# Optimization experiments

Measured on AMD Instinct MI355X. Metric: run time of the kernel, lower is better.

## Reference

```python
import jax, jax.numpy as jnp
import numpy as np
from jax import lax

PI = 3.141592653589793

def _sobel_kernel(dtype):
    # (2,1,3,3): channel 0 = d/dx (Sobel x), channel 1 = d/dy (Sobel y)
    sx = jnp.array([[-1., 0., 1.], [-2., 0., 2.], [-1., 0., 1.]], dtype=dtype)
    sy = jnp.array([[-1., -2., -1.], [0., 0., 0.], [1., 2., 1.]], dtype=dtype)
    return jnp.stack([sx, sy], axis=0)[:, None]

def _orientation_weights(dtype):
    # angles pi/8, 3pi/8, ..., 15pi/8 -> rows (cos, sin); last 2 rows = identity (copy dx, dy)
    angles = (2.0 * jnp.arange(8, dtype=dtype) + 1.0) * (PI / 8.0)
    basis = jnp.stack([jnp.cos(angles), jnp.sin(angles)], axis=1)  # (8,2)
    return jnp.concatenate([basis, jnp.eye(2, dtype=dtype)], axis=0)  # (10,2)

def setup_inputs() -> dict:
    key = jax.random.key(0)
    x = jax.random.normal(key, (1, 1, 4096, 4096), dtype=jnp.float32)
    return {"x": x}

def reference(x):
    dt = x.dtype
    # 1) image gradients via Sobel conv, pad 1 -> (1,2,H,W)
    grads = lax.conv_general_dilated(
        x, _sobel_kernel(dt), window_strides=(1, 1), padding=[(1, 1), (1, 1)],
        dimension_numbers=("NCHW", "OIHW", "NCHW"))
    # 2) 1x1 orientation conv: (10,2) basis dot product -> (1,10,H,W)
    W = _orientation_weights(dt)
    feats = jnp.einsum("oc,bchw->bohw", W, grads)
    cosines = feats[:, :8]        # (1,8,H,W)
    dx, dy = feats[:, 8], feats[:, 9]
    # 3) histogram layer: one-hot argmax over orientation fibre, weighted by |grad|
    mag = jnp.sqrt(dx * dx + dy * dy)                      # (1,H,W)
    idx = jnp.argmax(cosines, axis=1)                      # (1,H,W) int
    occupancy = jax.nn.one_hot(idx, 8, axis=1, dtype=dt)   # (1,8,H,W)
    hist = occupancy * mag[:, None]                        # (1,8,H,W)
    # 4) subgrid accumulation: depthwise 4x4 ones conv, pad 2 -> (1,8,H+1,W+1)
    ones_k = jnp.ones((8, 1, 4, 4), dtype=dt)
    out = lax.conv_general_dilated(
        hist, ones_k, window_strides=(1, 1), padding=[(2, 2), (2, 2)],
        dimension_numbers=("NCHW", "OIHW", "NCHW"), feature_group_count=8)
    return out
```

## Files before the change

kernel.cpp:

```cpp
#include <hip/hip_runtime.h>
#include <math.h>

#define N   4096
#define NO  4097
#define TO  32
#define GW  129

struct OrientCoef { float c[8]; float s[8]; };

__global__ __launch_bounds__(256, 4) void sift_fused(const float* __restrict__ x,
                                                     float* __restrict__ out,
                                                     OrientCoef cf) {
    int bid = blockIdx.y * GW + blockIdx.x;
    {
        const int nwg = GW * GW;
        const int q = nwg / 8, r = nwg % 8;
        int xcd = bid & 7, local = bid >> 3;
        bid = (xcd < r ? xcd * (q + 1) : r * (q + 1) + (xcd - r) * q) + local;
    }
    const int i0  = (bid / GW) * TO;
    const int j0  = (bid % GW) * TO;
    const int tid = threadIdx.x;

    __shared__ __align__(16) char smem[5040 + 8 * 35 * 32 * 4];
    float (*packed)[36]   = reinterpret_cast<float(*)[36]>(smem);
    float (*hsum)[35][32] = reinterpret_cast<float(*)[35][32]>(smem + 5040);
    float (*xs)[38]       = reinterpret_cast<float(*)[38]>(smem + 5040);

    for (int l = tid; l < 37 * 37; l += 256) {
        int lr = l / 37, lc = l % 37;
        int gr = i0 - 3 + lr, gc = j0 - 3 + lc;
        float v = 0.0f;
        if (gr >= 0 && gr < N && gc >= 0 && gc < N) v = x[(size_t)gr * N + gc];
        xs[lr][lc] = v;
    }
    __syncthreads();

    for (int l = tid; l < 35 * 35; l += 256) {
        int lr = l / 35, lc = l % 35;
        int gr = i0 - 2 + lr, gc = j0 - 2 + lc;
        float pv = 0.0f;
        if (gr >= 0 && gr < N && gc >= 0 && gc < N) {
            float x00 = xs[lr][lc],     x01 = xs[lr][lc + 1],     x02 = xs[lr][lc + 2];
            float x10 = xs[lr + 1][lc],                           x12 = xs[lr + 1][lc + 2];
            float x20 = xs[lr + 2][lc], x21 = xs[lr + 2][lc + 1], x22 = xs[lr + 2][lc + 2];
            float dx = (x02 - x00) + 2.0f * (x12 - x10) + (x22 - x20);
            float dy = (x20 - x00) + 2.0f * (x21 - x01) + (x22 - x02);
            float mag = sqrtf(dx * dx + dy * dy);
            int best = 0;
            float bv = fmaf(cf.s[0], dy, cf.c[0] * dx);
            #pragma unroll
            for (int o = 1; o < 8; ++o) {
                float cs = fmaf(cf.s[o], dy, cf.c[o] * dx);
                if (cs > bv) { bv = cs; best = o; }
            }
            pv = __uint_as_float((__float_as_uint(mag) & ~7u) | (unsigned)best);
        }
        packed[lr][lc] = pv;
    }
    __syncthreads();

    for (int l = tid; l < 35 * 32; l += 256) {
        int r = l / 32, jt = l % 32;
        float h[8] = {0.f, 0.f, 0.f, 0.f, 0.f, 0.f, 0.f, 0.f};
        #pragma unroll
        for (int w = 0; w < 4; ++w) {
            float m  = packed[r][jt + w];
            int   ii = (int)(__float_as_uint(m) & 7u);
            #pragma unroll
            for (int o = 0; o < 8; ++o)
                h[o] += (ii == o) ? m : 0.0f;
        }
        #pragma unroll
        for (int o = 0; o < 8; ++o) hsum[o][r][jt] = h[o];
    }
    __syncthreads();

    {
        const int o  = tid >> 5;
        const int jt = tid & 31;
        const int j  = j0 + jt;
        float r0 = hsum[o][0][jt];
        float r1 = hsum[o][1][jt];
        float r2 = hsum[o][2][jt];
        #pragma unroll 4
        for (int it = 0; it < 32; ++it) {
            float r3 = hsum[o][it + 3][jt];
            float s  = (r0 + r1) + (r2 + r3);
            int i = i0 + it;
            if (i < NO && j < NO)
                out[((size_t)o * NO + i) * NO + j] = s;
            r0 = r1; r1 = r2; r2 = r3;
        }
    }
}

extern "C" void kernel_launch(void* const* d_in, const int* in_sizes, int n_in,
                              void* d_out, int out_size, void* d_ws, size_t ws_size,
                              hipStream_t stream) {
    const float* x = (const float*)d_in[0];
    float* out = (float*)d_out;

    OrientCoef cf;
    const float pi8 = (float)(M_PI / 8.0);
    for (int o = 0; o < 8; ++o) {
        float angle = (float)(2 * o + 1) * pi8;
        cf.c[o] = (float)cos((double)angle);
        cf.s[o] = (float)sin((double)angle);
    }

    dim3 grid(GW, GW);
    sift_fused<<<grid, dim3(256), 0, stream>>>(x, out, cf);
}
```

Measured before the change: 686.1 us.

## Fuse horizontal and vertical box sums per orientation, drop hsum shared buffer

Removes the intermediate hsum shared-memory stage. Each thread now owns one orientation and one column and computes the horizontal 4-tap sum for its orientation directly from the packed tile, keeping a vertical sliding window in registers. This cuts shared memory use and one barrier, and launch bounds are raised to 8 blocks per CU for higher occupancy. In exchange, each thread redundantly reads packed values across the 8 orientations, and register pressure is tighter under the new bound.

```diff
diff --git a/kernel.cpp b/kernel.cpp
--- a/kernel.cpp
+++ b/kernel.cpp
@@ -8,7 +8,7 @@
 
 struct OrientCoef { float c[8]; float s[8]; };
 
-__global__ __launch_bounds__(256, 4) void sift_fused(const float* __restrict__ x,
+__global__ __launch_bounds__(256, 8) void sift_fused(const float* __restrict__ x,
                                                      float* __restrict__ out,
                                                      OrientCoef cf) {
     int bid = blockIdx.y * GW + blockIdx.x;
@@ -22,10 +22,8 @@
     const int j0  = (bid % GW) * TO;
     const int tid = threadIdx.x;
 
-    __shared__ __align__(16) char smem[5040 + 8 * 35 * 32 * 4];
-    float (*packed)[36]   = reinterpret_cast<float(*)[36]>(smem);
-    float (*hsum)[35][32] = reinterpret_cast<float(*)[35][32]>(smem + 5040);
-    float (*xs)[38]       = reinterpret_cast<float(*)[38]>(smem + 5040);
+    __shared__ float xs[37][38];
+    __shared__ float packed[35][36];
 
     for (int l = tid; l < 37 * 37; l += 256) {
         int lr = l / 37, lc = l % 37;
@@ -60,37 +58,29 @@
     }
     __syncthreads();
 
-    for (int l = tid; l < 35 * 32; l += 256) {
-        int r = l / 32, jt = l % 32;
-        float h[8] = {0.f, 0.f, 0.f, 0.f, 0.f, 0.f, 0.f, 0.f};
+    {
+        const int      o  = tid >> 5;
+        const int      jt = tid & 31;
+        const int      j  = j0 + jt;
+        const unsigned uo = (unsigned)o;
+        const bool     jok = (j < NO);
+        float* orow = out + ((size_t)o * NO + i0) * NO + j;
+        float w0 = 0.f, w1 = 0.f, w2 = 0.f;
         #pragma unroll
-        for (int w = 0; w < 4; ++w) {
-            float m  = packed[r][jt + w];
-            int   ii = (int)(__float_as_uint(m) & 7u);
-            #pragma unroll
-            for (int o = 0; o < 8; ++o)
-                h[o] += (ii == o) ? m : 0.0f;
-        }
-        #pragma unroll
-        for (int o = 0; o < 8; ++o) hsum[o][r][jt] = h[o];
-    }
-    __syncthreads();
-
-    {
-        const int o  = tid >> 5;
-        const int jt = tid & 31;
-        const int j  = j0 + jt;
-        float r0 = hsum[o][0][jt];
-        float r1 = hsum[o][1][jt];
-        float r2 = hsum[o][2][jt];
-        #pragma unroll 4
-        for (int it = 0; it < 32; ++it) {
-            float r3 = hsum[o][it + 3][jt];
-            float s  = (r0 + r1) + (r2 + r3);
-            int i = i0 + it;
-            if (i < NO && j < NO)
-                out[((size_t)o * NO + i) * NO + j] = s;
-            r0 = r1; r1 = r2; r2 = r3;
+        for (int r = 0; r < 35; ++r) {
+            float m0 = packed[r][jt],     m1 = packed[r][jt + 1];
+            float m2 = packed[r][jt + 2], m3 = packed[r][jt + 3];
+            float h = 0.f;
+            h += ((__float_as_uint(m0) & 7u) == uo) ? m0 : 0.f;
+            h += ((__float_as_uint(m1) & 7u) == uo) ? m1 : 0.f;
+            h += ((__float_as_uint(m2) & 7u) == uo) ? m2 : 0.f;
+            h += ((__float_as_uint(m3) & 7u) == uo) ? m3 : 0.f;
+            if (r >= 3) {
+                int i = i0 + r - 3;
+                if (jok && i < NO)
+                    orow[(size_t)(r - 3) * NO] = (w0 + w1) + (w2 + h);
+            }
+            w0 = w1; w1 = w2; w2 = h;
         }
     }
 }
```

Result: faster. 654.4 us (-4.6%).
